# Kernel tuning notes

Measured on AMD Instinct MI355X. Metric: run time of the kernel, lower is better.

The kernel has to match this reference:

```python
import jax, jax.numpy as jnp
import numpy as np

B, S, H, F, E, TOPK = 2, 1024, 1024, 2816, 8, 2

def setup_inputs() -> dict:
    key = jax.random.key(0)
    k1, k2, k3, k4 = jax.random.split(key, 4)
    return {
        "hidden_states": jax.random.normal(k1, (B, S, H), dtype=jnp.float32),
        "gate_w": jax.random.normal(k2, (E, H), dtype=jnp.float32) * 0.02,  # gate 1x1 conv == [E,H] matrix
        "w1": jax.random.normal(k3, (E, F, H), dtype=jnp.float32) * 0.02,   # per-expert up-proj
        "w2": jax.random.normal(k4, (E, H, F), dtype=jnp.float32) * 0.02,   # per-expert down-proj
        "top_k": TOPK,
    }

def reference(hidden_states, gate_w, w1, w2, top_k):
    b, s, h = hidden_states.shape
    e = gate_w.shape[0]
    x = hidden_states.reshape(-1, h)                       # [N, H]
    n = x.shape[0]
    # Router: 1x1 conv gate == linear, softmax, top-k, renormalize
    logits = x @ gate_w.T                                  # [N, E]
    probs = jax.nn.softmax(logits, axis=-1)
    topw, topi = jax.lax.top_k(probs, top_k)               # [N, k]
    topw = topw / jnp.sum(topw, axis=-1, keepdims=True)
    # Per-(token, expert) combine weight; zero for non-selected experts.
    # Equivalent to torch.where(topk_indices == e, topk_weights, 0).sum(-1).
    comb = jnp.zeros((n, e), dtype=x.dtype).at[jnp.arange(n)[:, None], topi].add(topw)  # [N, E]
    # Expert MLPs (1x1 convs == GEMMs): up -> SiLU -> down, weighted combine.
    up = jnp.einsum('nh,efh->nef', x, w1)                  # [N, E, F]
    act = jax.nn.silu(up)
    out = jnp.einsum('nef,ehf->neh', act, w2)              # [N, E, H]
    y = jnp.einsum('ne,neh->nh', comb, out)                # weighted combine
    return y.reshape(b, s, h)
```

## Files before the change

kernel.cpp:

```cpp
#include <hip/hip_runtime.h>
#include <stdint.h>

#define N_TOK 2048
#define H_DIM 1024
#define F_DIM 2816
#define N_EXP 8
#define NSLOT (N_TOK * 2)

#define BK 64
#define KSPLIT 2
#define KHALF (F_DIM / KSPLIT)

#define N8_X (N_TOK * H_DIM / 8)
#define N8_W (N_EXP * F_DIM * H_DIM / 8)

typedef __attribute__((ext_vector_type(8))) short bf16x8;
typedef __attribute__((ext_vector_type(4))) float f32x4;

typedef __attribute__((address_space(1))) unsigned int gu32;
typedef __attribute__((address_space(3))) unsigned int lu32;

static __device__ __forceinline__ unsigned short f2bf(float f) {
    union { float f; unsigned u; } v; v.f = f;
    unsigned r = v.u + 0x7fffu + ((v.u >> 16) & 1u);
    return (unsigned short)(r >> 16);
}

static __device__ __forceinline__ void gload16(const unsigned short* g, unsigned short* l) {
    __builtin_amdgcn_global_load_lds((const gu32*)g, (lu32*)l, 16, 0, 0);
}

__global__ __launch_bounds__(256) void convert_all_kernel(
    const float* __restrict__ x, const float* __restrict__ w1, const float* __restrict__ w2,
    unsigned short* __restrict__ x_bf, unsigned short* __restrict__ w1_bf, unsigned short* __restrict__ w2_bf)
{
    const int total = N8_X + 2 * N8_W;
    int i = blockIdx.x * 256 + threadIdx.x;
    const int stride = gridDim.x * 256;
    for (; i < total; i += stride) {
        const float* src; unsigned short* dst; size_t k;
        if (i < N8_X)            { src = x;  dst = x_bf;  k = i; }
        else if (i < N8_X + N8_W){ src = w1; dst = w1_bf; k = i - N8_X; }
        else                     { src = w2; dst = w2_bf; k = i - N8_X - N8_W; }
        const float4 a = *(const float4*)(src + k * 8);
        const float4 b = *(const float4*)(src + k * 8 + 4);
        ushort4 lo, hi;
        lo.x = f2bf(a.x); lo.y = f2bf(a.y); lo.z = f2bf(a.z); lo.w = f2bf(a.w);
        hi.x = f2bf(b.x); hi.y = f2bf(b.y); hi.z = f2bf(b.z); hi.w = f2bf(b.w);
        uint4 out;
        out.x = (unsigned)lo.x | ((unsigned)lo.y << 16);
        out.y = (unsigned)lo.z | ((unsigned)lo.w << 16);
        out.z = (unsigned)hi.x | ((unsigned)hi.y << 16);
        out.w = (unsigned)hi.z | ((unsigned)hi.w << 16);
        *(uint4*)(dst + k * 8) = out;
    }
}

__global__ __launch_bounds__(256) void router_kernel(
    const float* __restrict__ x, const float* __restrict__ gate_w,
    int* __restrict__ counts, int* __restrict__ row_token, float* __restrict__ row_weight,
    int* __restrict__ slot_e, int* __restrict__ slot_pos)
{
    __shared__ float gsm[N_EXP * H_DIM];
    for (int i = threadIdx.x; i < N_EXP * H_DIM; i += 256) gsm[i] = gate_w[i];
    __syncthreads();

    const int wave = threadIdx.x >> 6;
    const int lane = threadIdx.x & 63;
    const int n = blockIdx.x * 4 + wave;
    if (n >= N_TOK) return;

    float xv[16];
#pragma unroll
    for (int i = 0; i < 16; i++) xv[i] = x[(size_t)n * H_DIM + lane + 64 * i];

    float logit[N_EXP];
#pragma unroll
    for (int e = 0; e < N_EXP; e++) {
        float p = 0.f;
#pragma unroll
        for (int i = 0; i < 16; i++) p += xv[i] * gsm[e * H_DIM + lane + 64 * i];
#pragma unroll
        for (int s = 32; s > 0; s >>= 1) p += __shfl_xor(p, s, 64);
        logit[e] = p;
    }

    if (lane == 0) {
        int e0 = 0; float l0 = logit[0];
#pragma unroll
        for (int e = 1; e < N_EXP; e++) if (logit[e] > l0) { l0 = logit[e]; e0 = e; }
        int e1 = -1; float l1 = -3.4e38f;
#pragma unroll
        for (int e = 0; e < N_EXP; e++) if (e != e0 && logit[e] > l1) { l1 = logit[e]; e1 = e; }
        float w0 = 1.f / (1.f + __expf(l1 - l0));
        float w1 = 1.f - w0;
        int p0 = atomicAdd(&counts[e0], 1);
        int p1 = atomicAdd(&counts[e1], 1);
        row_token[e0 * N_TOK + p0] = n;  row_weight[e0 * N_TOK + p0] = w0;
        row_token[e1 * N_TOK + p1] = n;  row_weight[e1 * N_TOK + p1] = w1;
        slot_e[n * 2 + 0] = e0;  slot_pos[n * 2 + 0] = p0;
        slot_e[n * 2 + 1] = e1;  slot_pos[n * 2 + 1] = p1;
    }
}

__global__ void scan_kernel(const int* __restrict__ counts, int* __restrict__ offsets)
{
    if (threadIdx.x == 0 && blockIdx.x == 0) {
        int acc = 0;
        for (int e = 0; e < N_EXP; e++) { offsets[e] = acc; acc += counts[e]; }
    }
}

__global__ __launch_bounds__(256) void up_gemm_kernel(
    const unsigned short* __restrict__ x_bf, const unsigned short* __restrict__ w1_bf,
    const int* __restrict__ counts, const int* __restrict__ offsets,
    const int* __restrict__ row_token,
    unsigned short* __restrict__ act)
{
    const int e = blockIdx.z;
    const int cnt = counts[e];
    const int mTile = blockIdx.y;
    if (mTile * 128 >= cnt) return;
    const int fTile = blockIdx.x;
    const int off = offsets[e];

    __shared__ __align__(16) unsigned short As[128 * 64];
    __shared__ __align__(16) unsigned short Bs[128 * 64];

    const int tid = threadIdx.x;
    const int lane = tid & 63;
    const int wave = tid >> 6;
    const int wm = (wave >> 1) * 64, wn = (wave & 1) * 64;

    const unsigned short* aSrc[4];
    const unsigned short* bSrc[4];
#pragma unroll
    for (int j = 0; j < 4; j++) {
        const int row_local = wave * 32 + j * 8 + (lane >> 3);
        const int pos = mTile * 128 + row_local;
        const int tok = row_token[e * N_TOK + min(pos, cnt - 1)];
        aSrc[j] = x_bf + (size_t)tok * H_DIM + (lane & 7) * 8;
        bSrc[j] = w1_bf + ((size_t)e * F_DIM + fTile * 128 + row_local) * H_DIM + (lane & 7) * 8;
    }

    f32x4 acc[4][4];
#pragma unroll
    for (int i = 0; i < 4; i++)
#pragma unroll
        for (int j = 0; j < 4; j++) acc[i][j] = (f32x4)(0.f);

    const int NKT = H_DIM / BK;
    for (int kt = 0; kt < NKT; kt++) {
        const int koff = kt * BK;
#pragma unroll
        for (int j = 0; j < 4; j++) {
            gload16(aSrc[j] + koff, As + (wave * 4 + j) * 512);
            gload16(bSrc[j] + koff, Bs + (wave * 4 + j) * 512);
        }
        __syncthreads();
#pragma unroll
        for (int kk = 0; kk < BK / 32; kk++) {
            const int kloc = kk * 32 + (lane >> 4) * 8;
            bf16x8 af[4], bfr[4];
#pragma unroll
            for (int i = 0; i < 4; i++)
                af[i] = *(const bf16x8*)(As + (wm + i * 16 + (lane & 15)) * 64 + kloc);
#pragma unroll
            for (int i = 0; i < 4; i++)
                bfr[i] = *(const bf16x8*)(Bs + (wn + i * 16 + (lane & 15)) * 64 + kloc);
#pragma unroll
            for (int i = 0; i < 4; i++)
#pragma unroll
                for (int j = 0; j < 4; j++)
                    acc[i][j] = __builtin_amdgcn_mfma_f32_16x16x32_bf16(af[i], bfr[j], acc[i][j], 0, 0, 0);
        }
        __syncthreads();
    }

#pragma unroll
    for (int i = 0; i < 4; i++) {
        const int mrow = wm + i * 16 + ((lane >> 4) << 2);
#pragma unroll
        for (int r = 0; r < 4; r++) {
            const int m = mTile * 128 + mrow + r;
            if (m < cnt) {
#pragma unroll
                for (int j = 0; j < 4; j++) {
                    float v = acc[i][j][r];
                    float s = v / (1.f + __expf(-v));
                    int col = fTile * 128 + wn + j * 16 + (lane & 15);
                    act[(size_t)(off + m) * F_DIM + col] = f2bf(s);
                }
            }
        }
    }
}

__global__ __launch_bounds__(256) void down_gemm_kernel(
    const unsigned short* __restrict__ act, const unsigned short* __restrict__ w2_bf,
    const int* __restrict__ counts, const int* __restrict__ offsets,
    const float* __restrict__ row_weight,
    float* __restrict__ out_partial)
{
    const int e  = blockIdx.z & (N_EXP - 1);
    const int ks = blockIdx.z >> 3;
    const int cnt = counts[e];
    const int mTile = blockIdx.y;
    if (mTile * 128 >= cnt) return;
    const int hTile = blockIdx.x;
    const int off = offsets[e];
    const int kbase = ks * KHALF;

    __shared__ __align__(16) unsigned short As[128 * 64];
    __shared__ __align__(16) unsigned short Bs[128 * 64];

    const int tid = threadIdx.x;
    const int lane = tid & 63;
    const int wave = tid >> 6;
    const int wm = (wave >> 1) * 64, wn = (wave & 1) * 64;

    const unsigned short* aSrc[4];
    const unsigned short* bSrc[4];
#pragma unroll
    for (int j = 0; j < 4; j++) {
        const int row_local = wave * 32 + j * 8 + (lane >> 3);
        const int slot = off + min(mTile * 128 + row_local, cnt - 1);
        aSrc[j] = act + (size_t)slot * F_DIM + kbase + (lane & 7) * 8;
        bSrc[j] = w2_bf + ((size_t)e * H_DIM + hTile * 128 + row_local) * F_DIM + kbase + (lane & 7) * 8;
    }

    f32x4 acc[4][4];
#pragma unroll
    for (int i = 0; i < 4; i++)
#pragma unroll
        for (int j = 0; j < 4; j++) acc[i][j] = (f32x4)(0.f);

    const int NKT = KHALF / BK;
    for (int kt = 0; kt < NKT; kt++) {
        const int koff = kt * BK;
#pragma unroll
        for (int j = 0; j < 4; j++) {
            gload16(aSrc[j] + koff, As + (wave * 4 + j) * 512);
            gload16(bSrc[j] + koff, Bs + (wave * 4 + j) * 512);
        }
        __syncthreads();
#pragma unroll
        for (int kk = 0; kk < BK / 32; kk++) {
            const int kloc = kk * 32 + (lane >> 4) * 8;
            bf16x8 af[4], bfr[4];
#pragma unroll
            for (int i = 0; i < 4; i++)
                af[i] = *(const bf16x8*)(As + (wm + i * 16 + (lane & 15)) * 64 + kloc);
#pragma unroll
            for (int i = 0; i < 4; i++)
                bfr[i] = *(const bf16x8*)(Bs + (wn + i * 16 + (lane & 15)) * 64 + kloc);
#pragma unroll
            for (int i = 0; i < 4; i++)
#pragma unroll
                for (int j = 0; j < 4; j++)
                    acc[i][j] = __builtin_amdgcn_mfma_f32_16x16x32_bf16(af[i], bfr[j], acc[i][j], 0, 0, 0);
        }
        __syncthreads();
    }

    float* obase = out_partial + (size_t)ks * NSLOT * H_DIM;
#pragma unroll
    for (int i = 0; i < 4; i++) {
        const int mrow = wm + i * 16 + ((lane >> 4) << 2);
#pragma unroll
        for (int r = 0; r < 4; r++) {
            const int m = mTile * 128 + mrow + r;
            if (m < cnt) {
                const float w = row_weight[e * N_TOK + m];
#pragma unroll
                for (int j = 0; j < 4; j++) {
                    int col = hTile * 128 + wn + j * 16 + (lane & 15);
                    obase[(size_t)(off + m) * H_DIM + col] = w * acc[i][j][r];
                }
            }
        }
    }
}

__global__ __launch_bounds__(256) void combine_kernel(
    const float* __restrict__ out_partial, const int* __restrict__ offsets,
    const int* __restrict__ slot_e, const int* __restrict__ slot_pos,
    float* __restrict__ out)
{
    const int n = blockIdx.x;
    const int r0 = offsets[slot_e[n * 2 + 0]] + slot_pos[n * 2 + 0];
    const int r1 = offsets[slot_e[n * 2 + 1]] + slot_pos[n * 2 + 1];
    const int t = threadIdx.x;
    const float* p0 = out_partial;
    const float* p1 = out_partial + (size_t)NSLOT * H_DIM;
    const float4 a = *(const float4*)(p0 + (size_t)r0 * H_DIM + t * 4);
    const float4 b = *(const float4*)(p1 + (size_t)r0 * H_DIM + t * 4);
    const float4 c = *(const float4*)(p0 + (size_t)r1 * H_DIM + t * 4);
    const float4 d = *(const float4*)(p1 + (size_t)r1 * H_DIM + t * 4);
    float4 s;
    s.x = (a.x + b.x) + (c.x + d.x);
    s.y = (a.y + b.y) + (c.y + d.y);
    s.z = (a.z + b.z) + (c.z + d.z);
    s.w = (a.w + b.w) + (c.w + d.w);
    *(float4*)(out + (size_t)n * H_DIM + t * 4) = s;
}

extern "C" void kernel_launch(void* const* d_in, const int* in_sizes, int n_in,
                              void* d_out, int out_size, void* d_ws, size_t ws_size,
                              hipStream_t stream) {
    const float* x      = (const float*)d_in[0];
    const float* gate_w = (const float*)d_in[1];
    const float* w1     = (const float*)d_in[2];
    const float* w2     = (const float*)d_in[3];
    float* out = (float*)d_out;

    char* ws = (char*)d_ws;
    size_t o = 0;
    auto alloc = [&](size_t bytes) -> void* {
        void* p = ws + o;
        o = (o + bytes + 255) & ~(size_t)255;
        return p;
    };
    int*   counts     = (int*)  alloc(N_EXP * sizeof(int));
    int*   offsets    = (int*)  alloc(N_EXP * sizeof(int));
    int*   row_token  = (int*)  alloc((size_t)N_EXP * N_TOK * sizeof(int));
    float* row_weight = (float*)alloc((size_t)N_EXP * N_TOK * sizeof(float));
    int*   slot_e     = (int*)  alloc((size_t)N_TOK * 2 * sizeof(int));
    int*   slot_pos   = (int*)  alloc((size_t)N_TOK * 2 * sizeof(int));
    unsigned short* act = (unsigned short*)alloc((size_t)NSLOT * F_DIM * sizeof(unsigned short));
    float* out_partial = (float*)alloc((size_t)KSPLIT * NSLOT * H_DIM * sizeof(float));
    unsigned short* x_bf  = (unsigned short*)alloc((size_t)N_TOK * H_DIM * sizeof(unsigned short));
    unsigned short* w1_bf = (unsigned short*)alloc((size_t)N_EXP * F_DIM * H_DIM * sizeof(unsigned short));
    unsigned short* w2_bf = (unsigned short*)alloc((size_t)N_EXP * H_DIM * F_DIM * sizeof(unsigned short));

    hipMemsetAsync(counts, 0, N_EXP * sizeof(int), stream);

    router_kernel<<<N_TOK / 4, 256, 0, stream>>>(x, gate_w, counts, row_token, row_weight, slot_e, slot_pos);
    scan_kernel<<<1, 64, 0, stream>>>(counts, offsets);
    convert_all_kernel<<<2048, 256, 0, stream>>>(x, w1, w2, x_bf, w1_bf, w2_bf);
    up_gemm_kernel<<<dim3(F_DIM / 128, N_TOK / 128, N_EXP), 256, 0, stream>>>(
        x_bf, w1_bf, counts, offsets, row_token, act);
    down_gemm_kernel<<<dim3(H_DIM / 128, N_TOK / 128, N_EXP * KSPLIT), 256, 0, stream>>>(
        act, w2_bf, counts, offsets, row_weight, out_partial);
    combine_kernel<<<N_TOK, 256, 0, stream>>>(out_partial, offsets, slot_e, slot_pos, out);
}
```

Measured before the change: 391.7 us.

## Fuse MoE combine into down GEMM via atomic adds and four-way K split

The down-projection GEMM now scales each row by its routing weight and atomically adds it directly into the zeroed output at the token's row. This removes the partial-sum buffers, the slot bookkeeping and the separate combine kernel. The K split for the down GEMM rises from two to four to expose more parallelism, and the bf16 conversion loop is unrolled by two with a larger grid. The cost is more global float atomics, contention on shared output rows, and summation order that is no longer deterministic.

```diff
diff --git a/kernel.cpp b/kernel.cpp
--- a/kernel.cpp
+++ b/kernel.cpp
@@ -8,8 +8,8 @@
 #define NSLOT (N_TOK * 2)
 
 #define BK 64
-#define KSPLIT 2
-#define KHALF (F_DIM / KSPLIT)
+#define KSPLIT 4
+#define KPART (F_DIM / KSPLIT)
 
 #define N8_X (N_TOK * H_DIM / 8)
 #define N8_W (N_EXP * F_DIM * H_DIM / 8)
@@ -30,6 +30,28 @@
     __builtin_amdgcn_global_load_lds((const gu32*)g, (lu32*)l, 16, 0, 0);
 }
 
+static __device__ __forceinline__ void conv8(
+    const float* __restrict__ x, const float* __restrict__ w1, const float* __restrict__ w2,
+    unsigned short* __restrict__ x_bf, unsigned short* __restrict__ w1_bf, unsigned short* __restrict__ w2_bf,
+    int i)
+{
+    const float* src; unsigned short* dst; size_t k;
+    if (i < N8_X)            { src = x;  dst = x_bf;  k = i; }
+    else if (i < N8_X + N8_W){ src = w1; dst = w1_bf; k = i - N8_X; }
+    else                     { src = w2; dst = w2_bf; k = i - N8_X - N8_W; }
+    const float4 a = *(const float4*)(src + k * 8);
+    const float4 b = *(const float4*)(src + k * 8 + 4);
+    ushort4 lo, hi;
+    lo.x = f2bf(a.x); lo.y = f2bf(a.y); lo.z = f2bf(a.z); lo.w = f2bf(a.w);
+    hi.x = f2bf(b.x); hi.y = f2bf(b.y); hi.z = f2bf(b.z); hi.w = f2bf(b.w);
+    uint4 out;
+    out.x = (unsigned)lo.x | ((unsigned)lo.y << 16);
+    out.y = (unsigned)lo.z | ((unsigned)lo.w << 16);
+    out.z = (unsigned)hi.x | ((unsigned)hi.y << 16);
+    out.w = (unsigned)hi.z | ((unsigned)hi.w << 16);
+    *(uint4*)(dst + k * 8) = out;
+}
+
 __global__ __launch_bounds__(256) void convert_all_kernel(
     const float* __restrict__ x, const float* __restrict__ w1, const float* __restrict__ w2,
     unsigned short* __restrict__ x_bf, unsigned short* __restrict__ w1_bf, unsigned short* __restrict__ w2_bf)
@@ -37,29 +59,16 @@
     const int total = N8_X + 2 * N8_W;
     int i = blockIdx.x * 256 + threadIdx.x;
     const int stride = gridDim.x * 256;
-    for (; i < total; i += stride) {
-        const float* src; unsigned short* dst; size_t k;
-        if (i < N8_X)            { src = x;  dst = x_bf;  k = i; }
-        else if (i < N8_X + N8_W){ src = w1; dst = w1_bf; k = i - N8_X; }
-        else                     { src = w2; dst = w2_bf; k = i - N8_X - N8_W; }
-        const float4 a = *(const float4*)(src + k * 8);
-        const float4 b = *(const float4*)(src + k * 8 + 4);
-        ushort4 lo, hi;
-        lo.x = f2bf(a.x); lo.y = f2bf(a.y); lo.z = f2bf(a.z); lo.w = f2bf(a.w);
-        hi.x = f2bf(b.x); hi.y = f2bf(b.y); hi.z = f2bf(b.z); hi.w = f2bf(b.w);
-        uint4 out;
-        out.x = (unsigned)lo.x | ((unsigned)lo.y << 16);
-        out.y = (unsigned)lo.z | ((unsigned)lo.w << 16);
-        out.z = (unsigned)hi.x | ((unsigned)hi.y << 16);
-        out.w = (unsigned)hi.z | ((unsigned)hi.w << 16);
-        *(uint4*)(dst + k * 8) = out;
-    }
+    for (; i + stride < total; i += 2 * stride) {
+        conv8(x, w1, w2, x_bf, w1_bf, w2_bf, i);
+        conv8(x, w1, w2, x_bf, w1_bf, w2_bf, i + stride);
+    }
+    if (i < total) conv8(x, w1, w2, x_bf, w1_bf, w2_bf, i);
 }
 
 __global__ __launch_bounds__(256) void router_kernel(
     const float* __restrict__ x, const float* __restrict__ gate_w,
-    int* __restrict__ counts, int* __restrict__ row_token, float* __restrict__ row_weight,
-    int* __restrict__ slot_e, int* __restrict__ slot_pos)
+    int* __restrict__ counts, int* __restrict__ row_token, float* __restrict__ row_weight)
 {
     __shared__ float gsm[N_EXP * H_DIM];
     for (int i = threadIdx.x; i < N_EXP * H_DIM; i += 256) gsm[i] = gate_w[i];
@@ -98,8 +107,6 @@
         int p1 = atomicAdd(&counts[e1], 1);
         row_token[e0 * N_TOK + p0] = n;  row_weight[e0 * N_TOK + p0] = w0;
         row_token[e1 * N_TOK + p1] = n;  row_weight[e1 * N_TOK + p1] = w1;
-        slot_e[n * 2 + 0] = e0;  slot_pos[n * 2 + 0] = p0;
-        slot_e[n * 2 + 1] = e1;  slot_pos[n * 2 + 1] = p1;
     }
 }
 
@@ -199,8 +206,8 @@
 __global__ __launch_bounds__(256) void down_gemm_kernel(
     const unsigned short* __restrict__ act, const unsigned short* __restrict__ w2_bf,
     const int* __restrict__ counts, const int* __restrict__ offsets,
-    const float* __restrict__ row_weight,
-    float* __restrict__ out_partial)
+    const int* __restrict__ row_token, const float* __restrict__ row_weight,
+    float* __restrict__ out)
 {
     const int e  = blockIdx.z & (N_EXP - 1);
     const int ks = blockIdx.z >> 3;
@@ -209,7 +216,7 @@
     if (mTile * 128 >= cnt) return;
     const int hTile = blockIdx.x;
     const int off = offsets[e];
-    const int kbase = ks * KHALF;
+    const int kbase = ks * KPART;
 
     __shared__ __align__(16) unsigned short As[128 * 64];
     __shared__ __align__(16) unsigned short Bs[128 * 64];
@@ -235,7 +242,7 @@
 #pragma unroll
         for (int j = 0; j < 4; j++) acc[i][j] = (f32x4)(0.f);
 
-    const int NKT = KHALF / BK;
+    const int NKT = KPART / BK;
     for (int kt = 0; kt < NKT; kt++) {
         const int koff = kt * BK;
 #pragma unroll
@@ -263,7 +270,6 @@
         __syncthreads();
     }
 
-    float* obase = out_partial + (size_t)ks * NSLOT * H_DIM;
 #pragma unroll
     for (int i = 0; i < 4; i++) {
         const int mrow = wm + i * 16 + ((lane >> 4) << 2);
@@ -272,37 +278,15 @@
             const int m = mTile * 128 + mrow + r;
             if (m < cnt) {
                 const float w = row_weight[e * N_TOK + m];
+                const int n = row_token[e * N_TOK + m];
 #pragma unroll
                 for (int j = 0; j < 4; j++) {
                     int col = hTile * 128 + wn + j * 16 + (lane & 15);
-                    obase[(size_t)(off + m) * H_DIM + col] = w * acc[i][j][r];
+                    atomicAdd(out + (size_t)n * H_DIM + col, w * acc[i][j][r]);
                 }
             }
         }
     }
-}
-
-__global__ __launch_bounds__(256) void combine_kernel(
-    const float* __restrict__ out_partial, const int* __restrict__ offsets,
-    const int* __restrict__ slot_e, const int* __restrict__ slot_pos,
-    float* __restrict__ out)
-{
-    const int n = blockIdx.x;
-    const int r0 = offsets[slot_e[n * 2 + 0]] + slot_pos[n * 2 + 0];
-    const int r1 = offsets[slot_e[n * 2 + 1]] + slot_pos[n * 2 + 1];
-    const int t = threadIdx.x;
-    const float* p0 = out_partial;
-    const float* p1 = out_partial + (size_t)NSLOT * H_DIM;
-    const float4 a = *(const float4*)(p0 + (size_t)r0 * H_DIM + t * 4);
-    const float4 b = *(const float4*)(p1 + (size_t)r0 * H_DIM + t * 4);
-    const float4 c = *(const float4*)(p0 + (size_t)r1 * H_DIM + t * 4);
-    const float4 d = *(const float4*)(p1 + (size_t)r1 * H_DIM + t * 4);
-    float4 s;
-    s.x = (a.x + b.x) + (c.x + d.x);
-    s.y = (a.y + b.y) + (c.y + d.y);
-    s.z = (a.z + b.z) + (c.z + d.z);
-    s.w = (a.w + b.w) + (c.w + d.w);
-    *(float4*)(out + (size_t)n * H_DIM + t * 4) = s;
 }
 
 extern "C" void kernel_launch(void* const* d_in, const int* in_sizes, int n_in,
@@ -325,22 +309,19 @@
     int*   offsets    = (int*)  alloc(N_EXP * sizeof(int));
     int*   row_token  = (int*)  alloc((size_t)N_EXP * N_TOK * sizeof(int));
     float* row_weight = (float*)alloc((size_t)N_EXP * N_TOK * sizeof(float));
-    int*   slot_e     = (int*)  alloc((size_t)N_TOK * 2 * sizeof(int));
-    int*   slot_pos   = (int*)  alloc((size_t)N_TOK * 2 * sizeof(int));
     unsigned short* act = (unsigned short*)alloc((size_t)NSLOT * F_DIM * sizeof(unsigned short));
-    float* out_partial = (float*)alloc((size_t)KSPLIT * NSLOT * H_DIM * sizeof(float));
     unsigned short* x_bf  = (unsigned short*)alloc((size_t)N_TOK * H_DIM * sizeof(unsigned short));
     unsigned short* w1_bf = (unsigned short*)alloc((size_t)N_EXP * F_DIM * H_DIM * sizeof(unsigned short));
     unsigned short* w2_bf = (unsigned short*)alloc((size_t)N_EXP * H_DIM * F_DIM * sizeof(unsigned short));
 
     hipMemsetAsync(counts, 0, N_EXP * sizeof(int), stream);
-
-    router_kernel<<<N_TOK / 4, 256, 0, stream>>>(x, gate_w, counts, row_token, row_weight, slot_e, slot_pos);
+    hipMemsetAsync(out, 0, (size_t)N_TOK * H_DIM * sizeof(float), stream);
+
+    router_kernel<<<N_TOK / 4, 256, 0, stream>>>(x, gate_w, counts, row_token, row_weight);
     scan_kernel<<<1, 64, 0, stream>>>(counts, offsets);
-    convert_all_kernel<<<2048, 256, 0, stream>>>(x, w1, w2, x_bf, w1_bf, w2_bf);
+    convert_all_kernel<<<4096, 256, 0, stream>>>(x, w1, w2, x_bf, w1_bf, w2_bf);
     up_gemm_kernel<<<dim3(F_DIM / 128, N_TOK / 128, N_EXP), 256, 0, stream>>>(
         x_bf, w1_bf, counts, offsets, row_token, act);
     down_gemm_kernel<<<dim3(H_DIM / 128, N_TOK / 128, N_EXP * KSPLIT), 256, 0, stream>>>(
-        act, w2_bf, counts, offsets, row_weight, out_partial);
-    combine_kernel<<<N_TOK, 256, 0, stream>>>(out_partial, offsets, slot_e, slot_pos, out);
-}
+        act, w2_bf, counts, offsets, row_token, row_weight, out);
+}
```

New measurement: 431.6 us. 10.2% more time.
